# Performance work log

Hardware: AMD Instinct MI355X
Metric: run time of the kernel (lower is better)

## Reference

```python
import jax, jax.numpy as jnp
import numpy as np

N = 50000
E = 800000
NEG_SLOPE = 0.2


def setup_inputs() -> dict:
    key = jax.random.key(0)
    ks = jax.random.split(key, 12)
    feat = jax.random.normal(ks[0], (N, 256), dtype=jnp.float32)
    src = jax.random.randint(ks[1], (E,), 0, N, dtype=jnp.int32)
    dst = jax.random.randint(ks[2], (E,), 0, N, dtype=jnp.int32)
    # layer 1: in=256 -> H=4, D=64 (concat 256)
    W1 = jax.random.normal(ks[3], (256, 256), dtype=jnp.float32) * (1.0 / np.sqrt(256))
    attn_l1 = jax.random.normal(ks[4], (4, 64), dtype=jnp.float32) * 0.1
    attn_r1 = jax.random.normal(ks[5], (4, 64), dtype=jnp.float32) * 0.1
    bias1 = jnp.zeros((256,), dtype=jnp.float32)
    # layer 2: in=256 -> H=1, D=128
    W2 = jax.random.normal(ks[6], (256, 128), dtype=jnp.float32) * (1.0 / np.sqrt(256))
    attn_l2 = jax.random.normal(ks[7], (1, 128), dtype=jnp.float32) * 0.1
    attn_r2 = jax.random.normal(ks[8], (1, 128), dtype=jnp.float32) * 0.1
    bias2 = jnp.zeros((128,), dtype=jnp.float32)
    return {"feat": feat, "src": src, "dst": dst,
            "W1": W1, "attn_l1": attn_l1, "attn_r1": attn_r1, "bias1": bias1,
            "W2": W2, "attn_l2": attn_l2, "attn_r2": attn_r2, "bias2": bias2}


def gat_conv(feat, src, dst, W, attn_l, attn_r, bias, apply_relu):
    H, D = attn_l.shape
    n = feat.shape[0]
    ft = (feat @ W).reshape(n, H, D)                      # [N,H,D]
    el = jnp.einsum('nhd,hd->nh', ft, attn_l)             # [N,H]
    er = jnp.einsum('nhd,hd->nh', ft, attn_r)             # [N,H]
    e = el[src] + er[dst]                                 # [E,H]  u_add_v
    e = jnp.where(e > 0, e, NEG_SLOPE * e)                # leaky_relu
    # edge softmax grouped by dst
    m = jax.ops.segment_max(e, dst, num_segments=n)       # [N,H]
    ex = jnp.exp(e - m[dst])
    denom = jax.ops.segment_sum(ex, dst, num_segments=n)  # [N,H]
    a = ex / denom[dst]                                   # [E,H]
    msg = ft[src] * a[:, :, None]                         # [E,H,D]
    out = jax.ops.segment_sum(msg, dst, num_segments=n)   # [N,H,D]
    out = out + bias.reshape(1, H, D)
    out = out.reshape(n, H * D)                           # concat_out
    if apply_relu:
        out = jax.nn.relu(out)
    return out


def reference(feat, src, dst, W1, attn_l1, attn_r1, bias1, W2, attn_l2, attn_r2, bias2):
    h = gat_conv(feat, src, dst, W1, attn_l1, attn_r1, bias1, apply_relu=True)
    h = gat_conv(h, src, dst, W2, attn_l2, attn_r2, bias2, apply_relu=False)
    return h
```

## Files before the change

### kernel.cpp

```cpp
#include <hip/hip_runtime.h>

#define NEG_SLOPE 0.2f
#define SHARD_CAP 1024

typedef short s16x8 __attribute__((ext_vector_type(8)));
typedef float f32x4 __attribute__((ext_vector_type(4)));
typedef float f32x2 __attribute__((ext_vector_type(2)));
typedef unsigned int u32x4 __attribute__((ext_vector_type(4)));

typedef __attribute__((address_space(3))) unsigned int lds_u32;
typedef __attribute__((address_space(1))) const unsigned int glb_u32;

__device__ __forceinline__ unsigned short f2bf(float f) {
    unsigned int u = __float_as_uint(f);
    unsigned int r = (u + 0x7fffu + ((u >> 16) & 1u)) >> 16;
    return (unsigned short)r;
}
__device__ __forceinline__ float bf2f(unsigned int us) {
    return __uint_as_float(us << 16);
}

__device__ __forceinline__ u32x4 gload16(const char* p) {
    u32x4 r;
    asm volatile("global_load_dwordx4 %0, %1, off" : "=v"(r) : "v"(p));
    return r;
}


__global__ __launch_bounds__(256) void binpart_k(
        const int* __restrict__ src, const int* __restrict__ dst, int E,
        int* __restrict__ bin_cur, int* __restrict__ ovf_n,
        int2* __restrict__ pairs,
        int* __restrict__ ovf_dst, int* __restrict__ ovf_src,
        const float* __restrict__ W1, const float* __restrict__ al1,
        const float* __restrict__ ar1,
        const float* __restrict__ W2, const float* __restrict__ al2,
        const float* __restrict__ ar2,
        float* __restrict__ wl1, float* __restrict__ wl2,
        unsigned short* __restrict__ Bt1h, unsigned short* __restrict__ Bt1l,
        unsigned short* __restrict__ Bt2h, unsigned short* __restrict__ Bt2l) {
    const int b = blockIdx.x;
    if (b == 0) {
        int k = threadIdx.x;
        #pragma unroll
        for (int h = 0; h < 4; h++) {
            float sl = 0.f, sr = 0.f;
            #pragma unroll 8
            for (int d = 0; d < 64; d++) {
                float wv = W1[k * 256 + h * 64 + d];
                sl = fmaf(wv, al1[h * 64 + d], sl);
                sr = fmaf(wv, ar1[h * 64 + d], sr);
            }
            wl1[k * 8 + h] = sl;
            wl1[k * 8 + 4 + h] = sr;
        }
        float sl = 0.f, sr = 0.f;
        #pragma unroll 8
        for (int d = 0; d < 128; d++) {
            float wv = W2[k * 128 + d];
            sl = fmaf(wv, al2[d], sl);
            sr = fmaf(wv, ar2[d], sr);
        }
        wl2[k * 2 + 0] = sl;
        wl2[k * 2 + 1] = sr;
        return;
    }
    if (b <= 4) {
        int c = (b - 1) * 64 + (threadIdx.x >> 2);
        int kq = threadIdx.x & 3;
        #pragma unroll 8
        for (int kk = 0; kk < 64; kk++) {
            int k = kq + kk * 4;
            float w = W1[k * 256 + c];
            unsigned short h = f2bf(w);
            unsigned short l = f2bf(w - bf2f(h));
            Bt1h[c * 256 + k] = h;
            Bt1l[c * 256 + k] = l;
        }
        return;
    }
    if (b <= 6) {
        int c = (b - 5) * 64 + (threadIdx.x >> 2);
        int kq = threadIdx.x & 3;
        #pragma unroll 8
        for (int kk = 0; kk < 64; kk++) {
            int k = kq + kk * 4;
            float w = W2[k * 128 + c];
            unsigned short h = f2bf(w);
            unsigned short l = f2bf(w - bf2f(h));
            Bt2h[c * 256 + k] = h;
            Bt2l[c * 256 + k] = l;
        }
        return;
    }
    __shared__ int l_cnt[256];
    __shared__ int l_base[256];
    const int tid = threadIdx.x;
    const int pb = b - 7;
    const int shard = pb & 7;
    const int base_e = pb * 2048 + tid * 8;
    int s[8], d[8], bn[8], rk[8];
    bool v[8];
    if (base_e + 7 < E) {
        int4 a0 = *(const int4*)(src + base_e);
        int4 a1 = *(const int4*)(src + base_e + 4);
        int4 c0 = *(const int4*)(dst + base_e);
        int4 c1 = *(const int4*)(dst + base_e + 4);
        s[0]=a0.x; s[1]=a0.y; s[2]=a0.z; s[3]=a0.w;
        s[4]=a1.x; s[5]=a1.y; s[6]=a1.z; s[7]=a1.w;
        d[0]=c0.x; d[1]=c0.y; d[2]=c0.z; d[3]=c0.w;
        d[4]=c1.x; d[5]=c1.y; d[6]=c1.z; d[7]=c1.w;
        #pragma unroll
        for (int i = 0; i < 8; i++) v[i] = true;
    } else {
        #pragma unroll
        for (int i = 0; i < 8; i++) {
            int e = base_e + i;
            v[i] = e < E;
            s[i] = v[i] ? src[e] : 0;
            d[i] = v[i] ? dst[e] : 0;
        }
    }
    l_cnt[tid] = 0;
    __syncthreads();
    #pragma unroll
    for (int i = 0; i < 8; i++) {
        bn[i] = d[i] >> 8;
        if (v[i]) rk[i] = atomicAdd(&l_cnt[bn[i]], 1);
    }
    __syncthreads();
    {
        int c = l_cnt[tid];
        if (c > 0) l_base[tid] = atomicAdd(&bin_cur[(tid * 8 + shard) * 16], c);
    }
    __syncthreads();
    #pragma unroll
    for (int i = 0; i < 8; i++) {
        if (v[i]) {
            int pos = l_base[bn[i]] + rk[i];
            if (pos < SHARD_CAP) {
                int2 p; p.x = s[i]; p.y = d[i];
                pairs[(((size_t)bn[i] * 8 + shard) << 10) + pos] = p;
            } else {
                int j = atomicAdd(ovf_n, 1);
                ovf_dst[j] = d[i]; ovf_src[j] = s[i];
            }
        }
    }
}


__global__ __launch_bounds__(256) void prepfill_k(
        const int* __restrict__ bin_cur, const int2* __restrict__ pairs,
        int* __restrict__ cnt, int* __restrict__ bucket,
        int* __restrict__ ovf_n, int* __restrict__ ovf_dst, int* __restrict__ ovf_src,
        const float* __restrict__ feat, const float* __restrict__ wl1,
        unsigned short* __restrict__ Ah, unsigned short* __restrict__ Al,
        float* __restrict__ el1, float* __restrict__ er1, int Nn, int nbin) {
    if ((int)blockIdx.x < nbin) {
        __shared__ int l_cnt[256];
        const int b = blockIdx.x;
        const int tid = threadIdx.x;
        l_cnt[tid] = 0;
        __syncthreads();
        #pragma unroll
        for (int sh = 0; sh < 8; sh++) {
            const int ec = min(bin_cur[(b * 8 + sh) * 16], SHARD_CAP);
            const int2* pp = pairs + (((size_t)b * 8 + sh) << 10);
            for (int i = tid; i < ec; i += 256) {
                int2 p = pp[i];
                int pos = atomicAdd(&l_cnt[p.y & 255], 1);
                if (pos < 64) bucket[((size_t)p.y << 6) + pos] = p.x;
                else {
                    int j = atomicAdd(ovf_n, 1);
                    ovf_dst[j] = p.y; ovf_src[j] = p.x;
                }
            }
        }
        __syncthreads();
        int node = b * 256 + tid;
        if (node < Nn) cnt[node] = l_cnt[tid];
        return;
    }
    const int lane = threadIdx.x & 63, wid = threadIdx.x >> 6;
    const int n = ((int)blockIdx.x - nbin) * 4 + wid;
    if (n >= Nn) return;
    float4 f = ((const float4*)(feat + (size_t)n * 256))[lane];
    unsigned short h0 = f2bf(f.x), h1 = f2bf(f.y), h2 = f2bf(f.z), h3 = f2bf(f.w);
    unsigned short l0 = f2bf(f.x - bf2f(h0)), l1 = f2bf(f.y - bf2f(h1));
    unsigned short l2 = f2bf(f.z - bf2f(h2)), l3 = f2bf(f.w - bf2f(h3));
    uint2 hv, lv;
    hv.x = (unsigned)h0 | ((unsigned)h1 << 16);
    hv.y = (unsigned)h2 | ((unsigned)h3 << 16);
    lv.x = (unsigned)l0 | ((unsigned)l1 << 16);
    lv.y = (unsigned)l2 | ((unsigned)l3 << 16);
    ((uint2*)(Ah + (size_t)n * 256))[lane] = hv;
    ((uint2*)(Al + (size_t)n * 256))[lane] = lv;

    float ff[4] = {f.x, f.y, f.z, f.w};
    float pa[4] = {0.f, 0.f, 0.f, 0.f}, pb[4] = {0.f, 0.f, 0.f, 0.f};
    const float* wp = wl1 + lane * 32;
    #pragma unroll
    for (int j = 0; j < 4; j++) {
        float4 wa = *(const float4*)(wp + j * 8);
        float4 wb = *(const float4*)(wp + j * 8 + 4);
        pa[0] = fmaf(ff[j], wa.x, pa[0]); pa[1] = fmaf(ff[j], wa.y, pa[1]);
        pa[2] = fmaf(ff[j], wa.z, pa[2]); pa[3] = fmaf(ff[j], wa.w, pa[3]);
        pb[0] = fmaf(ff[j], wb.x, pb[0]); pb[1] = fmaf(ff[j], wb.y, pb[1]);
        pb[2] = fmaf(ff[j], wb.z, pb[2]); pb[3] = fmaf(ff[j], wb.w, pb[3]);
    }
    #pragma unroll
    for (int h = 0; h < 4; h++) {
        #pragma unroll
        for (int o = 32; o > 0; o >>= 1) {
            pa[h] += __shfl_xor(pa[h], o);
            pb[h] += __shfl_xor(pb[h], o);
        }
    }
    if (lane == 0) {
        ((float4*)el1)[n] = float4{pa[0], pa[1], pa[2], pa[3]};
        ((float4*)er1)[n] = float4{pb[0], pb[1], pb[2], pb[3]};
    }
}


__global__ __launch_bounds__(256) void gemm_k(const unsigned short* __restrict__ Ah,
                                              const unsigned short* __restrict__ Al,
                                              const unsigned short* __restrict__ Bh,
                                              const unsigned short* __restrict__ Bl,
                                              unsigned short* __restrict__ Cb,
                                              int M, int Nc) {
    __shared__ __align__(16) unsigned short SB[12288];

    const int tid = threadIdx.x;
    const int lane = tid & 63, wid = tid >> 6;
    const int row0 = blockIdx.y * 128;
    const int col0 = blockIdx.x * 64;
    const int wm = (wid & 1) * 64;
    const int wn = (wid >> 1) * 32;
    const int quad = lane >> 4, mrow = lane & 15;

    const unsigned short* gb[6];
    unsigned ldsoff[6];
    {
        const int lr = lane >> 2;
        const int kc = (lane & 3) * 8;
        #pragma unroll
        for (int j = 0; j < 6; j++) {
            int c = wid * 6 + j;
            const unsigned short* base;
            int row;
            if (c < 8)       { base = Ah; row = min(row0 + c * 16 + lr, M - 1); }
            else if (c < 16) { base = Al; row = min(row0 + (c - 8) * 16 + lr, M - 1); }
            else if (c < 20) { base = Bh; row = col0 + (c - 16) * 16 + lr; }
            else             { base = Bl; row = col0 + (c - 20) * 16 + lr; }
            gb[j] = base + (size_t)row * 256 + kc;
            ldsoff[j] = (unsigned)c * 512;
        }
    }

    f32x4 acc[4][2];
    #pragma unroll
    for (int i = 0; i < 4; i++)
        #pragma unroll
        for (int j = 0; j < 2; j++) acc[i][j] = f32x4{0.f, 0.f, 0.f, 0.f};

    for (int kt = 0; kt < 8; kt++) {
        __syncthreads();
        #pragma unroll
        for (int j = 0; j < 6; j++) {
            __builtin_amdgcn_global_load_lds((glb_u32*)(gb[j] + kt * 32),
                                             (lds_u32*)&SB[ldsoff[j]], 16, 0, 0);
        }
        __syncthreads();

        s16x8 ah[4], al4[4], bh[2], bl[2];
        #pragma unroll
        for (int i = 0; i < 4; i++) {
            int r = wm + 16 * i + mrow;
            ah[i]  = *(const s16x8*)&SB[r * 32 + quad * 8];
            al4[i] = *(const s16x8*)&SB[4096 + r * 32 + quad * 8];
        }
        #pragma unroll
        for (int j = 0; j < 2; j++) {
            int r = wn + 16 * j + mrow;
            bh[j] = *(const s16x8*)&SB[8192 + r * 32 + quad * 8];
            bl[j] = *(const s16x8*)&SB[10240 + r * 32 + quad * 8];
        }
        #pragma unroll
        for (int i = 0; i < 4; i++)
            #pragma unroll
            for (int j = 0; j < 2; j++) {
                acc[i][j] = __builtin_amdgcn_mfma_f32_16x16x32_bf16(ah[i],  bh[j], acc[i][j], 0, 0, 0);
                acc[i][j] = __builtin_amdgcn_mfma_f32_16x16x32_bf16(ah[i],  bl[j], acc[i][j], 0, 0, 0);
                acc[i][j] = __builtin_amdgcn_mfma_f32_16x16x32_bf16(al4[i], bh[j], acc[i][j], 0, 0, 0);
            }
    }

    #pragma unroll
    for (int i = 0; i < 4; i++) {
        #pragma unroll
        for (int j = 0; j < 2; j++) {
            int col = col0 + wn + 16 * j + mrow;
            int rbase = row0 + wm + 16 * i + quad * 4;
            #pragma unroll
            for (int r = 0; r < 4; r++) {
                int row = rbase + r;
                if (row < M) Cb[(size_t)row * Nc + col] = f2bf(acc[i][j][r]);
            }
        }
    }
}


__device__ __forceinline__ void fma8(f32x2* acc, float wgt, u32x4 u) {
    f32x2 w2; w2.x = wgt; w2.y = wgt;
    f32x2 p;
    p.x = __uint_as_float(u.x << 16); p.y = __uint_as_float(u.x & 0xffff0000u);
    acc[0] = p * w2 + acc[0];
    p.x = __uint_as_float(u.y << 16); p.y = __uint_as_float(u.y & 0xffff0000u);
    acc[1] = p * w2 + acc[1];
    p.x = __uint_as_float(u.z << 16); p.y = __uint_as_float(u.z & 0xffff0000u);
    acc[2] = p * w2 + acc[2];
    p.x = __uint_as_float(u.w << 16); p.y = __uint_as_float(u.w & 0xffff0000u);
    acc[3] = p * w2 + acc[3];
}

template <int H, int D, bool RELU, bool FUSE2>
__global__ __launch_bounds__(256) void fagg_k(const unsigned short* __restrict__ ft,
                                              const float* __restrict__ el,
                                              const float* __restrict__ er,
                                              const int* __restrict__ cnt,
                                              const int* __restrict__ bucket,
                                              const int* __restrict__ ovf_n,
                                              const int* __restrict__ ovf_dst,
                                              const int* __restrict__ ovf_src,
                                              const float* __restrict__ bias,
                                              float* __restrict__ out, int n_nodes,
                                              unsigned short* __restrict__ oh,
                                              unsigned short* __restrict__ ol,
                                              const float* __restrict__ wl2,
                                              float* __restrict__ el2,
                                              float* __restrict__ er2) {
    constexpr int HD = H * D;
    constexpr int LPE = HD / 8;
    constexpr int EPI = 64 / LPE;
    constexpr int SH = (HD == 256) ? 9 : 8;
    const int lane = threadIdx.x & 63;
    const int w = threadIdx.x >> 6;
    const int n = blockIdx.x * 4 + w;
    __shared__ int   s_src[4][64];
    __shared__ float s_a[4][64 * H];
    if (n >= n_nodes) return;
    const int deg = cnt[n];
    const int novf = *ovf_n;
    const int lane_sub = lane & (LPE - 1);
    const int q = lane / LPE;
    const int c0 = lane_sub * 8;
    const int h_of = c0 / D;
    const unsigned lsub16 = (unsigned)(lane_sub * 16);
    const char* fb = (const char*)ft;
    const char* eb = (const char*)el;

    float ern[H];
    #pragma unroll
    for (int h = 0; h < H; h++) ern[h] = er[n * H + h];

    f32x2 acc[4];
    #pragma unroll
    for (int t = 0; t < 4; t++) acc[t] = f32x2{0.f, 0.f};

    const int* s_src_w = s_src[w];
    const float* s_a_w = s_a[w];

#define GADDR(i) (fb + (((unsigned)s_src_w[(i) * EPI + q] << SH) + lsub16))
#define WT(i)    (s_a_w[((i) * EPI + q) * H + h_of])

    if (deg <= 64 && novf == 0) {
        const bool act = lane < deg;
        int sv = act ? bucket[(n << 6) + lane] : 0;
        s_src[w][lane] = sv;
        float evr[H];
        if constexpr (H == 4) {
            float4 e4 = *(const float4*)(eb + ((unsigned)sv << 4));
            evr[0] = e4.x; evr[1] = e4.y; evr[2] = e4.z; evr[3] = e4.w;
        } else {
            evr[0] = *(const float*)(eb + ((unsigned)sv << 2));
        }
        const int nl = (deg + EPI - 1) / EPI;
        u32x4 v0 = gload16(GADDR(0)), v1 = gload16(GADDR(1));
        u32x4 v2 = gload16(GADDR(2)), v3 = gload16(GADDR(3));
        u32x4 v4 = gload16(GADDR(4)), v5 = gload16(GADDR(5));
        u32x4 v6 = gload16(GADDR(6)), v7 = gload16(GADDR(7));
        float ex[H], sm[H];
        #pragma unroll
        for (int h = 0; h < H; h++) {
            float t = evr[h] + ern[h];
            t = t > 0.f ? t : NEG_SLOPE * t;
            ex[h] = act ? __expf(t) : 0.f;
            sm[h] = ex[h];
        }
        #pragma unroll
        for (int h = 0; h < H; h++)
            for (int o = 32; o > 0; o >>= 1) sm[h] += __shfl_xor(sm[h], o);
        #pragma unroll
        for (int h = 0; h < H; h++)
            s_a[w][lane * H + h] = ex[h] * (sm[h] > 0.f ? 1.f / sm[h] : 0.f);
        asm volatile("s_waitcnt vmcnt(0)" ::: "memory");
        __builtin_amdgcn_sched_barrier(0);
        fma8(acc, WT(0), v0); fma8(acc, WT(1), v1);
        fma8(acc, WT(2), v2); fma8(acc, WT(3), v3);
        fma8(acc, WT(4), v4); fma8(acc, WT(5), v5);
        fma8(acc, WT(6), v6); fma8(acc, WT(7), v7);
        constexpr int MAXNL = 64 / EPI;
        #pragma unroll
        for (int i0 = 8; i0 < MAXNL; i0 += 4) {
            if (i0 >= nl) break;
            u32x4 a  = *(const u32x4*)GADDR(i0);
            u32x4 b2 = *(const u32x4*)GADDR(i0 + 1);
            u32x4 c2 = *(const u32x4*)GADDR(i0 + 2);
            u32x4 d2 = *(const u32x4*)GADDR(i0 + 3);
            fma8(acc, WT(i0), a);      fma8(acc, WT(i0 + 1), b2);
            fma8(acc, WT(i0 + 2), c2); fma8(acc, WT(i0 + 3), d2);
        }
    } else {
        const int bval = deg < 64 ? deg : 64;
        const bool act = lane < bval;
        int sv0 = act ? bucket[(n << 6) + lane] : 0;
        s_src[w][lane] = sv0;
        float sm[H];
        #pragma unroll
        for (int h = 0; h < H; h++) sm[h] = 0.f;
        {
            float evr[H];
            if constexpr (H == 4) {
                float4 e4 = ((const float4*)el)[sv0];
                evr[0] = e4.x; evr[1] = e4.y; evr[2] = e4.z; evr[3] = e4.w;
            } else evr[0] = el[sv0];
            #pragma unroll
            for (int h = 0; h < H; h++) {
                float t = evr[h] + ern[h];
                t = t > 0.f ? t : NEG_SLOPE * t;
                if (act) sm[h] += __expf(t);
            }
        }
        for (int i = lane; i < novf; i += 64) {
            if (ovf_dst[i] == n) {
                int sv = ovf_src[i];
                float evr[H];
                if constexpr (H == 4) {
                    float4 e4 = ((const float4*)el)[sv];
                    evr[0] = e4.x; evr[1] = e4.y; evr[2] = e4.z; evr[3] = e4.w;
                } else evr[0] = el[sv];
                #pragma unroll
                for (int h = 0; h < H; h++) {
                    float t = evr[h] + ern[h];
                    t = t > 0.f ? t : NEG_SLOPE * t;
                    sm[h] += __expf(t);
                }
            }
        }
        #pragma unroll
        for (int h = 0; h < H; h++)
            for (int o = 32; o > 0; o >>= 1) sm[h] += __shfl_xor(sm[h], o);
        float inv[H];
        #pragma unroll
        for (int h = 0; h < H; h++) inv[h] = (sm[h] > 0.f) ? (1.f / sm[h]) : 0.f;
        {
            float evr[H];
            if constexpr (H == 4) {
                float4 e4 = ((const float4*)el)[sv0];
                evr[0] = e4.x; evr[1] = e4.y; evr[2] = e4.z; evr[3] = e4.w;
            } else evr[0] = el[sv0];
            #pragma unroll
            for (int h = 0; h < H; h++) {
                float t = evr[h] + ern[h];
                t = t > 0.f ? t : NEG_SLOPE * t;
                s_a[w][lane * H + h] = act ? __expf(t) * inv[h] : 0.f;
            }
        }
        for (int e = q; e < 64; e += EPI) {
            unsigned bo = ((unsigned)s_src_w[e] << SH) + lsub16;
            u32x4 v = *(const u32x4*)(fb + bo);
            fma8(acc, s_a_w[e * H + h_of], v);
        }
        for (int i = 0; i < novf; i++) {
            if (ovf_dst[i] != n) continue;
            int sv = ovf_src[i];
            float elh, ernh, invh;
            if constexpr (H == 4) {
                float4 e4 = ((const float4*)el)[sv];
                elh  = (h_of & 2) ? ((h_of & 1) ? e4.w : e4.z)
                                  : ((h_of & 1) ? e4.y : e4.x);
                ernh = (h_of & 2) ? ((h_of & 1) ? ern[3] : ern[2])
                                  : ((h_of & 1) ? ern[1] : ern[0]);
                invh = (h_of & 2) ? ((h_of & 1) ? inv[3] : inv[2])
                                  : ((h_of & 1) ? inv[1] : inv[0]);
            } else {
                elh = el[sv]; ernh = ern[0]; invh = inv[0];
            }
            float t = elh + ernh;
            t = t > 0.f ? t : NEG_SLOPE * t;
            float wt = __expf(t) * invh;
            u32x4 v = *(const u32x4*)(fb + (((unsigned)sv << SH) + lsub16));
            if (q == 0) fma8(acc, wt, v);
        }
    }
#undef GADDR
#undef WT

    float accs[8];
    #pragma unroll
    for (int t = 0; t < 8; t++) accs[t] = acc[t >> 1][t & 1];

    #pragma unroll
    for (int t = 0; t < 8; t++) {
        #pragma unroll
        for (int s = LPE; s < 64; s <<= 1) accs[t] += __shfl_xor(accs[t], s);
    }
    if (lane < LPE) {
        float4 b0 = ((const float4*)bias)[lane * 2];
        float4 b1 = ((const float4*)bias)[lane * 2 + 1];
        float v[8] = {accs[0] + b0.x, accs[1] + b0.y, accs[2] + b0.z, accs[3] + b0.w,
                      accs[4] + b1.x, accs[5] + b1.y, accs[6] + b1.z, accs[7] + b1.w};
        if (RELU) {
            #pragma unroll
            for (int t = 0; t < 8; t++) v[t] = fmaxf(v[t], 0.f);
        }
        if constexpr (FUSE2) {
            unsigned short hh[8], ll[8];
            #pragma unroll
            for (int t = 0; t < 8; t++) {
                hh[t] = f2bf(v[t]);
                ll[t] = f2bf(v[t] - bf2f(hh[t]));
            }
            uint4 hv, lv;
            hv.x = (unsigned)hh[0] | ((unsigned)hh[1] << 16);
            hv.y = (unsigned)hh[2] | ((unsigned)hh[3] << 16);
            hv.z = (unsigned)hh[4] | ((unsigned)hh[5] << 16);
            hv.w = (unsigned)hh[6] | ((unsigned)hh[7] << 16);
            lv.x = (unsigned)ll[0] | ((unsigned)ll[1] << 16);
            lv.y = (unsigned)ll[2] | ((unsigned)ll[3] << 16);
            lv.z = (unsigned)ll[4] | ((unsigned)ll[5] << 16);
            lv.w = (unsigned)ll[6] | ((unsigned)ll[7] << 16);
            ((uint4*)(oh + (size_t)n * HD))[lane] = hv;
            ((uint4*)(ol + (size_t)n * HD))[lane] = lv;
            float pa = 0.f, pb = 0.f;
            #pragma unroll
            for (int t = 0; t < 8; t++) {
                float2 wv = ((const float2*)wl2)[lane * 8 + t];
                pa = fmaf(v[t], wv.x, pa);
                pb = fmaf(v[t], wv.y, pb);
            }
            #pragma unroll
            for (int o = 16; o > 0; o >>= 1) {
                pa += __shfl_xor(pa, o);
                pb += __shfl_xor(pb, o);
            }
            if (lane == 0) { el2[n] = pa; er2[n] = pb; }
        } else {
            float4 o0{v[0], v[1], v[2], v[3]};
            float4 o1{v[4], v[5], v[6], v[7]};
            float4* op = (float4*)out + (size_t)n * (HD / 4) + lane * 2;
            op[0] = o0;
            op[1] = o1;
        }
    }
}


extern "C" void kernel_launch(void* const* d_in, const int* in_sizes, int n_in,
                              void* d_out, int out_size, void* d_ws, size_t ws_size,
                              hipStream_t stream) {
    const float* feat    = (const float*)d_in[0];
    const int*   src     = (const int*)d_in[1];
    const int*   dst     = (const int*)d_in[2];
    const float* W1      = (const float*)d_in[3];
    const float* attn_l1 = (const float*)d_in[4];
    const float* attn_r1 = (const float*)d_in[5];
    const float* bias1   = (const float*)d_in[6];
    const float* W2      = (const float*)d_in[7];
    const float* attn_l2 = (const float*)d_in[8];
    const float* attn_r2 = (const float*)d_in[9];
    const float* bias2   = (const float*)d_in[10];
    float* out = (float*)d_out;

    const int N = in_sizes[0] / 256;
    const int E = in_sizes[1];
    const int nbin = (N + 255) >> 8;
    const int nbP = (E + 2047) / 2048;

    char* ws = (char*)d_ws;
    size_t o = 0;
    auto alloc = [&](size_t bytes) -> void* {
        void* p = ws + o;
        o = (o + bytes + 255) & ~(size_t)255;
        return p;
    };
    int* bin_cur = (int*)alloc(((size_t)nbin * 8 * 16 + 64) * 4);
    int* ovf_n   = bin_cur + (size_t)nbin * 8 * 16;
    int* cnt     = (int*)alloc((size_t)N * 4);
    int* bucket  = (int*)alloc((size_t)N * 64 * 4);
    int* ovf_dst = (int*)alloc((size_t)E * 4);
    int* ovf_src = (int*)alloc((size_t)E * 4);
    float* wl1 = (float*)alloc(256 * 8 * 4);
    float* wl2 = (float*)alloc(256 * 2 * 4);
    float* el1 = (float*)alloc((size_t)N * 4 * 4);
    float* er1 = (float*)alloc((size_t)N * 4 * 4);
    float* el2 = (float*)alloc((size_t)N * 4);
    float* er2 = (float*)alloc((size_t)N * 4);
    unsigned short* ft1b = (unsigned short*)alloc((size_t)N * 256 * 2);
    unsigned short* Ah   = (unsigned short*)alloc((size_t)N * 256 * 2);
    unsigned short* Al   = (unsigned short*)alloc((size_t)N * 256 * 2);
    unsigned short* Bt1h = (unsigned short*)alloc((size_t)256 * 256 * 2);
    unsigned short* Bt1l = (unsigned short*)alloc((size_t)256 * 256 * 2);
    unsigned short* Bt2h = (unsigned short*)alloc((size_t)128 * 256 * 2);
    unsigned short* Bt2l = (unsigned short*)alloc((size_t)128 * 256 * 2);
    unsigned short* ft2b = ft1b;
    unsigned short* h1h  = Ah;
    unsigned short* h1l  = Al;
    int2* pairs = (int2*)ft1b;

    hipMemsetAsync(bin_cur, 0, ((size_t)nbin * 8 * 16 + 64) * 4, stream);
    binpart_k<<<7 + nbP, 256, 0, stream>>>(src, dst, E, bin_cur, ovf_n, pairs,
                                           ovf_dst, ovf_src,
                                           W1, attn_l1, attn_r1, W2, attn_l2, attn_r2,
                                           wl1, wl2, Bt1h, Bt1l, Bt2h, Bt2l);
    prepfill_k<<<nbin + (N + 3) / 4, 256, 0, stream>>>(bin_cur, pairs, cnt, bucket,
                                                       ovf_n, ovf_dst, ovf_src,
                                                       feat, wl1, Ah, Al, el1, er1, N, nbin);

    gemm_k<<<dim3(4, (N + 127) / 128), 256, 0, stream>>>(Ah, Al, Bt1h, Bt1l, ft1b, N, 256);
    fagg_k<4, 64, true, true><<<(N + 3) / 4, 256, 0, stream>>>(ft1b, el1, er1, cnt, bucket,
                                                               ovf_n, ovf_dst, ovf_src,
                                                               bias1, nullptr, N,
                                                               h1h, h1l, wl2, el2, er2);

    gemm_k<<<dim3(2, (N + 127) / 128), 256, 0, stream>>>(h1h, h1l, Bt2h, Bt2l, ft2b, N, 128);
    fagg_k<1, 128, false, false><<<(N + 3) / 4, 256, 0, stream>>>(ft2b, el2, er2, cnt, bucket,
                                                                  ovf_n, ovf_dst, ovf_src,
                                                                  bias2, out, N,
                                                                  nullptr, nullptr, nullptr,
                                                                  nullptr, nullptr);
}
```

Before: 343.8 us.

## Process two destination nodes per wavefront in aggregation kernel using half-waves

The aggregation kernel now assigns two destination nodes per 64-lane wavefront, each handled by a 32-lane half, when both nodes have degree at most 32. This halves the grid size and is meant to cut wasted lanes, since the average in-degree is about 16 and most 64-wide slots would sit idle. Higher-degree pairs fall back to a serial per-node loop over the full wave. The epilogue is factored into a helper, and the inline-asm loads with an explicit vmcnt wait are replaced by plain loads. The trade-offs are the extra shuffles, the max-degree coupling between the two halves, and a slower fallback path for pairs with a high-degree node.

```diff
diff --git a/kernel.cpp b/kernel.cpp
--- a/kernel.cpp
+++ b/kernel.cpp
@@ -18,12 +18,6 @@
 }
 __device__ __forceinline__ float bf2f(unsigned int us) {
     return __uint_as_float(us << 16);
-}
-
-__device__ __forceinline__ u32x4 gload16(const char* p) {
-    u32x4 r;
-    asm volatile("global_load_dwordx4 %0, %1, off" : "=v"(r) : "v"(p));
-    return r;
 }
 
 
@@ -324,6 +318,66 @@
     acc[2] = p * w2 + acc[2];
     p.x = __uint_as_float(u.w << 16); p.y = __uint_as_float(u.w & 0xffff0000u);
     acc[3] = p * w2 + acc[3];
+}
+
+template <int H, int D, bool RELU, bool FUSE2>
+__device__ __forceinline__ void epi_node(
+        int n, const float* accs, int li, bool active, bool lead,
+        const float* __restrict__ bias, float* __restrict__ out,
+        unsigned short* __restrict__ oh, unsigned short* __restrict__ ol,
+        const float* __restrict__ wl2, float* __restrict__ el2,
+        float* __restrict__ er2) {
+    constexpr int HD = H * D;
+    float4 b0 = ((const float4*)bias)[li * 2];
+    float4 b1 = ((const float4*)bias)[li * 2 + 1];
+    float v[8] = {accs[0] + b0.x, accs[1] + b0.y, accs[2] + b0.z, accs[3] + b0.w,
+                  accs[4] + b1.x, accs[5] + b1.y, accs[6] + b1.z, accs[7] + b1.w};
+    if (RELU) {
+        #pragma unroll
+        for (int t = 0; t < 8; t++) v[t] = fmaxf(v[t], 0.f);
+    }
+    if constexpr (FUSE2) {
+        unsigned short hh[8], ll[8];
+        #pragma unroll
+        for (int t = 0; t < 8; t++) {
+            hh[t] = f2bf(v[t]);
+            ll[t] = f2bf(v[t] - bf2f(hh[t]));
+        }
+        uint4 hv, lv;
+        hv.x = (unsigned)hh[0] | ((unsigned)hh[1] << 16);
+        hv.y = (unsigned)hh[2] | ((unsigned)hh[3] << 16);
+        hv.z = (unsigned)hh[4] | ((unsigned)hh[5] << 16);
+        hv.w = (unsigned)hh[6] | ((unsigned)hh[7] << 16);
+        lv.x = (unsigned)ll[0] | ((unsigned)ll[1] << 16);
+        lv.y = (unsigned)ll[2] | ((unsigned)ll[3] << 16);
+        lv.z = (unsigned)ll[4] | ((unsigned)ll[5] << 16);
+        lv.w = (unsigned)ll[6] | ((unsigned)ll[7] << 16);
+        if (active) {
+            ((uint4*)(oh + (size_t)n * HD))[li] = hv;
+            ((uint4*)(ol + (size_t)n * HD))[li] = lv;
+        }
+        float pa = 0.f, pb = 0.f;
+        #pragma unroll
+        for (int t = 0; t < 8; t++) {
+            float2 wv = ((const float2*)wl2)[li * 8 + t];
+            pa = fmaf(v[t], wv.x, pa);
+            pb = fmaf(v[t], wv.y, pb);
+        }
+        #pragma unroll
+        for (int o = 16; o > 0; o >>= 1) {
+            pa += __shfl_xor(pa, o);
+            pb += __shfl_xor(pb, o);
+        }
+        if (lead) { el2[n] = pa; er2[n] = pb; }
+    } else {
+        if (active) {
+            float4 o0{v[0], v[1], v[2], v[3]};
+            float4 o1{v[4], v[5], v[6], v[7]};
+            float4* op = (float4*)out + (size_t)n * (HD / 4) + li * 2;
+            op[0] = o0;
+            op[1] = o1;
+        }
+    }
 }
 
 template <int H, int D, bool RELU, bool FUSE2>
@@ -344,41 +398,39 @@
                                               float* __restrict__ er2) {
     constexpr int HD = H * D;
     constexpr int LPE = HD / 8;
-    constexpr int EPI = 64 / LPE;
+    constexpr int EPIL = 32 / LPE;
+    constexpr int EPI_F = 64 / LPE;
     constexpr int SH = (HD == 256) ? 9 : 8;
     const int lane = threadIdx.x & 63;
     const int w = threadIdx.x >> 6;
-    const int n = blockIdx.x * 4 + w;
+    const int half = lane >> 5;
+    const int l32 = lane & 31;
+    const int nbase = blockIdx.x * 8 + w * 2;
     __shared__ int   s_src[4][64];
     __shared__ float s_a[4][64 * H];
-    if (n >= n_nodes) return;
-    const int deg = cnt[n];
+    if (nbase >= n_nodes) return;
+    const int n = nbase + half;
+    const bool nv = n < n_nodes;
+    const int deg = nv ? cnt[n] : 0;
     const int novf = *ovf_n;
     const int lane_sub = lane & (LPE - 1);
-    const int q = lane / LPE;
-    const int c0 = lane_sub * 8;
-    const int h_of = c0 / D;
+    const int h_of = (lane_sub * 8) / D;
     const unsigned lsub16 = (unsigned)(lane_sub * 16);
     const char* fb = (const char*)ft;
     const char* eb = (const char*)el;
 
-    float ern[H];
-    #pragma unroll
-    for (int h = 0; h < H; h++) ern[h] = er[n * H + h];
-
-    f32x2 acc[4];
-    #pragma unroll
-    for (int t = 0; t < 4; t++) acc[t] = f32x2{0.f, 0.f};
+    const int degw = max(deg, __shfl_xor(deg, 32));
 
     const int* s_src_w = s_src[w];
     const float* s_a_w = s_a[w];
 
-#define GADDR(i) (fb + (((unsigned)s_src_w[(i) * EPI + q] << SH) + lsub16))
-#define WT(i)    (s_a_w[((i) * EPI + q) * H + h_of])
-
-    if (deg <= 64 && novf == 0) {
-        const bool act = lane < deg;
-        int sv = act ? bucket[(n << 6) + lane] : 0;
+    if (degw <= 32 && novf == 0) {
+        const int q = l32 / LPE;
+        float ern[H];
+        #pragma unroll
+        for (int h = 0; h < H; h++) ern[h] = nv ? er[n * H + h] : 0.f;
+        const bool act = nv && (l32 < deg);
+        int sv = act ? bucket[(n << 6) + l32] : 0;
         s_src[w][lane] = sv;
         float evr[H];
         if constexpr (H == 4) {
@@ -387,11 +439,6 @@
         } else {
             evr[0] = *(const float*)(eb + ((unsigned)sv << 2));
         }
-        const int nl = (deg + EPI - 1) / EPI;
-        u32x4 v0 = gload16(GADDR(0)), v1 = gload16(GADDR(1));
-        u32x4 v2 = gload16(GADDR(2)), v3 = gload16(GADDR(3));
-        u32x4 v4 = gload16(GADDR(4)), v5 = gload16(GADDR(5));
-        u32x4 v6 = gload16(GADDR(6)), v7 = gload16(GADDR(7));
         float ex[H], sm[H];
         #pragma unroll
         for (int h = 0; h < H; h++) {
@@ -402,20 +449,32 @@
         }
         #pragma unroll
         for (int h = 0; h < H; h++)
-            for (int o = 32; o > 0; o >>= 1) sm[h] += __shfl_xor(sm[h], o);
+            for (int o = 16; o > 0; o >>= 1) sm[h] += __shfl_xor(sm[h], o);
         #pragma unroll
         for (int h = 0; h < H; h++)
             s_a[w][lane * H + h] = ex[h] * (sm[h] > 0.f ? 1.f / sm[h] : 0.f);
-        asm volatile("s_waitcnt vmcnt(0)" ::: "memory");
-        __builtin_amdgcn_sched_barrier(0);
+
+        f32x2 acc[4];
+        #pragma unroll
+        for (int t = 0; t < 4; t++) acc[t] = f32x2{0.f, 0.f};
+
+#define SLOT(i)  (half * 32 + (i) * EPIL + q)
+#define GADDR(i) (fb + (((unsigned)s_src_w[SLOT(i)] << SH) + lsub16))
+#define WT(i)    (s_a_w[SLOT(i) * H + h_of])
+        u32x4 v0 = *(const u32x4*)GADDR(0), v1 = *(const u32x4*)GADDR(1);
+        u32x4 v2 = *(const u32x4*)GADDR(2), v3 = *(const u32x4*)GADDR(3);
+        u32x4 v4 = *(const u32x4*)GADDR(4), v5 = *(const u32x4*)GADDR(5);
+        u32x4 v6 = *(const u32x4*)GADDR(6), v7 = *(const u32x4*)GADDR(7);
         fma8(acc, WT(0), v0); fma8(acc, WT(1), v1);
         fma8(acc, WT(2), v2); fma8(acc, WT(3), v3);
         fma8(acc, WT(4), v4); fma8(acc, WT(5), v5);
         fma8(acc, WT(6), v6); fma8(acc, WT(7), v7);
-        constexpr int MAXNL = 64 / EPI;
-        #pragma unroll
-        for (int i0 = 8; i0 < MAXNL; i0 += 4) {
-            if (i0 >= nl) break;
+        int nl = (deg + EPIL - 1) / EPIL;
+        int nlw = max(nl, __shfl_xor(nl, 32));
+        constexpr int MAXR = 32 / EPIL;
+        #pragma unroll
+        for (int i0 = 8; i0 < MAXR; i0 += 4) {
+            if (i0 >= nlw) break;
             u32x4 a  = *(const u32x4*)GADDR(i0);
             u32x4 b2 = *(const u32x4*)GADDR(i0 + 1);
             u32x4 c2 = *(const u32x4*)GADDR(i0 + 2);
@@ -423,147 +482,124 @@
             fma8(acc, WT(i0), a);      fma8(acc, WT(i0 + 1), b2);
             fma8(acc, WT(i0 + 2), c2); fma8(acc, WT(i0 + 3), d2);
         }
+#undef SLOT
+#undef GADDR
+#undef WT
+        float accs[8];
+        #pragma unroll
+        for (int t = 0; t < 8; t++) accs[t] = acc[t >> 1][t & 1];
+        #pragma unroll
+        for (int t = 0; t < 8; t++) {
+            #pragma unroll
+            for (int s = LPE; s < 32; s <<= 1) accs[t] += __shfl_xor(accs[t], s);
+        }
+        epi_node<H, D, RELU, FUSE2>(n, accs, lane & (LPE - 1),
+                                    nv && (l32 < LPE), nv && (l32 == 0),
+                                    bias, out, oh, ol, wl2, el2, er2);
     } else {
-        const int bval = deg < 64 ? deg : 64;
-        const bool act = lane < bval;
-        int sv0 = act ? bucket[(n << 6) + lane] : 0;
-        s_src[w][lane] = sv0;
-        float sm[H];
-        #pragma unroll
-        for (int h = 0; h < H; h++) sm[h] = 0.f;
-        {
-            float evr[H];
-            if constexpr (H == 4) {
-                float4 e4 = ((const float4*)el)[sv0];
-                evr[0] = e4.x; evr[1] = e4.y; evr[2] = e4.z; evr[3] = e4.w;
-            } else evr[0] = el[sv0];
-            #pragma unroll
-            for (int h = 0; h < H; h++) {
-                float t = evr[h] + ern[h];
-                t = t > 0.f ? t : NEG_SLOPE * t;
-                if (act) sm[h] += __expf(t);
-            }
-        }
-        for (int i = lane; i < novf; i += 64) {
-            if (ovf_dst[i] == n) {
-                int sv = ovf_src[i];
+        const int q_F = lane / LPE;
+        for (int si = 0; si < 2; si++) {
+            int nn = nbase + si;
+            if (nn >= n_nodes) break;
+            int dg = cnt[nn];
+            float ern[H];
+            #pragma unroll
+            for (int h = 0; h < H; h++) ern[h] = er[nn * H + h];
+            const int bval = dg < 64 ? dg : 64;
+            const bool act = lane < bval;
+            int sv0 = act ? bucket[(nn << 6) + lane] : 0;
+            s_src[w][lane] = sv0;
+            float sm[H];
+            #pragma unroll
+            for (int h = 0; h < H; h++) sm[h] = 0.f;
+            {
                 float evr[H];
                 if constexpr (H == 4) {
-                    float4 e4 = ((const float4*)el)[sv];
+                    float4 e4 = ((const float4*)el)[sv0];
                     evr[0] = e4.x; evr[1] = e4.y; evr[2] = e4.z; evr[3] = e4.w;
-                } else evr[0] = el[sv];
+                } else evr[0] = el[sv0];
                 #pragma unroll
                 for (int h = 0; h < H; h++) {
                     float t = evr[h] + ern[h];
                     t = t > 0.f ? t : NEG_SLOPE * t;
-                    sm[h] += __expf(t);
+                    if (act) sm[h] += __expf(t);
                 }
             }
-        }
-        #pragma unroll
-        for (int h = 0; h < H; h++)
-            for (int o = 32; o > 0; o >>= 1) sm[h] += __shfl_xor(sm[h], o);
-        float inv[H];
-        #pragma unroll
-        for (int h = 0; h < H; h++) inv[h] = (sm[h] > 0.f) ? (1.f / sm[h]) : 0.f;
-        {
-            float evr[H];
-            if constexpr (H == 4) {
-                float4 e4 = ((const float4*)el)[sv0];
-                evr[0] = e4.x; evr[1] = e4.y; evr[2] = e4.z; evr[3] = e4.w;
-            } else evr[0] = el[sv0];
-            #pragma unroll
-            for (int h = 0; h < H; h++) {
-                float t = evr[h] + ern[h];
+            for (int i = lane; i < novf; i += 64) {
+                if (ovf_dst[i] == nn) {
+                    int sv = ovf_src[i];
+                    float evr[H];
+                    if constexpr (H == 4) {
+                        float4 e4 = ((const float4*)el)[sv];
+                        evr[0] = e4.x; evr[1] = e4.y; evr[2] = e4.z; evr[3] = e4.w;
+                    } else evr[0] = el[sv];
+                    #pragma unroll
+                    for (int h = 0; h < H; h++) {
+                        float t = evr[h] + ern[h];
+                        t = t > 0.f ? t : NEG_SLOPE * t;
+                        sm[h] += __expf(t);
+                    }
+                }
+            }
+            #pragma unroll
+            for (int h = 0; h < H; h++)
+                for (int o = 32; o > 0; o >>= 1) sm[h] += __shfl_xor(sm[h], o);
+            float inv[H];
+            #pragma unroll
+            for (int h = 0; h < H; h++) inv[h] = (sm[h] > 0.f) ? (1.f / sm[h]) : 0.f;
+            {
+                float evr[H];
+                if constexpr (H == 4) {
+                    float4 e4 = ((const float4*)el)[sv0];
+                    evr[0] = e4.x; evr[1] = e4.y; evr[2] = e4.z; evr[3] = e4.w;
+                } else evr[0] = el[sv0];
+                #pragma unroll
+                for (int h = 0; h < H; h++) {
+                    float t = evr[h] + ern[h];
+                    t = t > 0.f ? t : NEG_SLOPE * t;
+                    s_a[w][lane * H + h] = act ? __expf(t) * inv[h] : 0.f;
+                }
+            }
+            f32x2 acc[4];
+            #pragma unroll
+            for (int t = 0; t < 4; t++) acc[t] = f32x2{0.f, 0.f};
+            for (int e = q_F; e < 64; e += EPI_F) {
+                unsigned bo = ((unsigned)s_src_w[e] << SH) + lsub16;
+                u32x4 v = *(const u32x4*)(fb + bo);
+                fma8(acc, s_a_w[e * H + h_of], v);
+            }
+            for (int i = 0; i < novf; i++) {
+                if (ovf_dst[i] != nn) continue;
+                int sv = ovf_src[i];
+                float elh, ernh, invh;
+                if constexpr (H == 4) {
+                    float4 e4 = ((const float4*)el)[sv];
+                    elh  = (h_of & 2) ? ((h_of & 1) ? e4.w : e4.z)
+                                      : ((h_of & 1) ? e4.y : e4.x);
+                    ernh = (h_of & 2) ? ((h_of & 1) ? ern[3] : ern[2])
+                                      : ((h_of & 1) ? ern[1] : ern[0]);
+                    invh = (h_of & 2) ? ((h_of & 1) ? inv[3] : inv[2])
+                                      : ((h_of & 1) ? inv[1] : inv[0]);
+                } else {
+                    elh = el[sv]; ernh = ern[0]; invh = inv[0];
+                }
+                float t = elh + ernh;
                 t = t > 0.f ? t : NEG_SLOPE * t;
-                s_a[w][lane * H + h] = act ? __expf(t) * inv[h] : 0.f;
-            }
-        }
-        for (int e = q; e < 64; e += EPI) {
-            unsigned bo = ((unsigned)s_src_w[e] << SH) + lsub16;
-            u32x4 v = *(const u32x4*)(fb + bo);
-            fma8(acc, s_a_w[e * H + h_of], v);
-        }
-        for (int i = 0; i < novf; i++) {
-            if (ovf_dst[i] != n) continue;
-            int sv = ovf_src[i];
-            float elh, ernh, invh;
-            if constexpr (H == 4) {
-                float4 e4 = ((const float4*)el)[sv];
-                elh  = (h_of & 2) ? ((h_of & 1) ? e4.w : e4.z)
-                                  : ((h_of & 1) ? e4.y : e4.x);
-                ernh = (h_of & 2) ? ((h_of & 1) ? ern[3] : ern[2])
-                                  : ((h_of & 1) ? ern[1] : ern[0]);
-                invh = (h_of & 2) ? ((h_of & 1) ? inv[3] : inv[2])
-                                  : ((h_of & 1) ? inv[1] : inv[0]);
-            } else {
-                elh = el[sv]; ernh = ern[0]; invh = inv[0];
-            }
-            float t = elh + ernh;
-            t = t > 0.f ? t : NEG_SLOPE * t;
-            float wt = __expf(t) * invh;
-            u32x4 v = *(const u32x4*)(fb + (((unsigned)sv << SH) + lsub16));
-            if (q == 0) fma8(acc, wt, v);
-        }
-    }
-#undef GADDR
-#undef WT
-
-    float accs[8];
-    #pragma unroll
-    for (int t = 0; t < 8; t++) accs[t] = acc[t >> 1][t & 1];
-
-    #pragma unroll
-    for (int t = 0; t < 8; t++) {
-        #pragma unroll
-        for (int s = LPE; s < 64; s <<= 1) accs[t] += __shfl_xor(accs[t], s);
-    }
-    if (lane < LPE) {
-        float4 b0 = ((const float4*)bias)[lane * 2];
-        float4 b1 = ((const float4*)bias)[lane * 2 + 1];
-        float v[8] = {accs[0] + b0.x, accs[1] + b0.y, accs[2] + b0.z, accs[3] + b0.w,
-                      accs[4] + b1.x, accs[5] + b1.y, accs[6] + b1.z, accs[7] + b1.w};
-        if (RELU) {
-            #pragma unroll
-            for (int t = 0; t < 8; t++) v[t] = fmaxf(v[t], 0.f);
-        }
-        if constexpr (FUSE2) {
-            unsigned short hh[8], ll[8];
+                float wt = __expf(t) * invh;
+                u32x4 v = *(const u32x4*)(fb + (((unsigned)sv << SH) + lsub16));
+                if (q_F == 0) fma8(acc, wt, v);
+            }
+            float accs[8];
+            #pragma unroll
+            for (int t = 0; t < 8; t++) accs[t] = acc[t >> 1][t & 1];
             #pragma unroll
             for (int t = 0; t < 8; t++) {
-                hh[t] = f2bf(v[t]);
-                ll[t] = f2bf(v[t] - bf2f(hh[t]));
-            }
-            uint4 hv, lv;
-            hv.x = (unsigned)hh[0] | ((unsigned)hh[1] << 16);
-            hv.y = (unsigned)hh[2] | ((unsigned)hh[3] << 16);
-            hv.z = (unsigned)hh[4] | ((unsigned)hh[5] << 16);
-            hv.w = (unsigned)hh[6] | ((unsigned)hh[7] << 16);
-            lv.x = (unsigned)ll[0] | ((unsigned)ll[1] << 16);
-            lv.y = (unsigned)ll[2] | ((unsigned)ll[3] << 16);
-            lv.z = (unsigned)ll[4] | ((unsigned)ll[5] << 16);
-            lv.w = (unsigned)ll[6] | ((unsigned)ll[7] << 16);
-            ((uint4*)(oh + (size_t)n * HD))[lane] = hv;
-            ((uint4*)(ol + (size_t)n * HD))[lane] = lv;
-            float pa = 0.f, pb = 0.f;
-            #pragma unroll
-            for (int t = 0; t < 8; t++) {
-                float2 wv = ((const float2*)wl2)[lane * 8 + t];
-                pa = fmaf(v[t], wv.x, pa);
-                pb = fmaf(v[t], wv.y, pb);
-            }
-            #pragma unroll
-            for (int o = 16; o > 0; o >>= 1) {
-                pa += __shfl_xor(pa, o);
-                pb += __shfl_xor(pb, o);
-            }
-            if (lane == 0) { el2[n] = pa; er2[n] = pb; }
-        } else {
-            float4 o0{v[0], v[1], v[2], v[3]};
-            float4 o1{v[4], v[5], v[6], v[7]};
-            float4* op = (float4*)out + (size_t)n * (HD / 4) + lane * 2;
-            op[0] = o0;
-            op[1] = o1;
+                #pragma unroll
+                for (int s = LPE; s < 64; s <<= 1) accs[t] += __shfl_xor(accs[t], s);
+            }
+            epi_node<H, D, RELU, FUSE2>(nn, accs, lane & (LPE - 1),
+                                        lane < LPE, lane == 0,
+                                        bias, out, oh, ol, wl2, el2, er2);
         }
     }
 }
@@ -631,13 +667,13 @@
                                                        feat, wl1, Ah, Al, el1, er1, N, nbin);
 
     gemm_k<<<dim3(4, (N + 127) / 128), 256, 0, stream>>>(Ah, Al, Bt1h, Bt1l, ft1b, N, 256);
-    fagg_k<4, 64, true, true><<<(N + 3) / 4, 256, 0, stream>>>(ft1b, el1, er1, cnt, bucket,
+    fagg_k<4, 64, true, true><<<(N + 7) / 8, 256, 0, stream>>>(ft1b, el1, er1, cnt, bucket,
                                                                ovf_n, ovf_dst, ovf_src,
                                                                bias1, nullptr, N,
                                                                h1h, h1l, wl2, el2, er2);
 
     gemm_k<<<dim3(2, (N + 127) / 128), 256, 0, stream>>>(h1h, h1l, Bt2h, Bt2l, ft2b, N, 128);
-    fagg_k<1, 128, false, false><<<(N + 3) / 4, 256, 0, stream>>>(ft2b, el2, er2, cnt, bucket,
+    fagg_k<1, 128, false, false><<<(N + 7) / 8, 256, 0, stream>>>(ft2b, el2, er2, cnt, bucket,
                                                                   ovf_n, ovf_dst, ovf_src,
                                                                   bias2, out, N,
                                                                   nullptr, nullptr, nullptr,
```

Result: slower. 355.5 us (+3.4%).
